# Kernel tuning notes

Measured on AMD Instinct MI355X. Metric: run time of the kernel, lower is better.

## Reference

```python
import jax, jax.numpy as jnp
import numpy as np

E = 8      # num routed experts
H = 1024   # hidden_size
I = 1408   # moe_intermediate_size
T = 2048   # tokens (batch*seq flattened)
K = 2      # top_k experts per token


def setup_inputs() -> dict:
    key = jax.random.key(0)
    k1, k2, k3, k4, k5 = jax.random.split(key, 5)
    x = jax.random.normal(k1, (T, H), dtype=jnp.float32)
    expert_ids = jax.random.randint(k2, (T, K), 0, E, dtype=jnp.int64)
    routing_weights = jax.random.uniform(k3, (T, K), dtype=jnp.float32)
    # kaiming_uniform_(a=sqrt(5)) on 2D tensor -> bound = 1/sqrt(fan_in), fan_in = dim1
    b1 = 1.0 / np.sqrt(2 * I)
    w1 = jax.random.uniform(k4, (E * H, 2 * I), dtype=jnp.float32, minval=-b1, maxval=b1)
    b2 = 1.0 / np.sqrt(H)
    w2 = jax.random.uniform(k5, (E * I, H), dtype=jnp.float32, minval=-b2, maxval=b2)
    return {"x": x, "expert_ids": expert_ids, "routing_weights": routing_weights,
            "w1": w1, "w2": w2}


def reference(x, expert_ids, routing_weights, w1, w2):
    # Fused routed MLP: per token, for each of its top-k experts e with gate p:
    #   out += p * (silu(x @ W1_gate[e]) * (x @ W1_up[e])) @ W2[e]
    w1r = w1.reshape(E, H, 2 * I)   # fused gate+up per expert
    w2r = w2.reshape(E, I, H)       # down proj per expert

    h = jnp.einsum('th,ehi->eti', x, w1r)           # [E, T, 2I]
    gate, up = h[..., :I], h[..., I:]
    act = jax.nn.silu(gate) * up                    # [E, T, I]
    y = jnp.einsum('eti,eih->eth', act, w2r)        # [E, T, H]

    # combine weights: [T, E] = sum over the k slots of onehot(expert)*routing_weight
    disp = jnp.sum(jax.nn.one_hot(expert_ids, E, dtype=x.dtype)
                   * routing_weights[..., None], axis=1)  # [T, E]
    out = jnp.einsum('eth,te->th', y, disp)         # [T, H]
    return out
```

## Files before the change

### kernel.cpp

```cpp
#include <hip/hip_runtime.h>
#include <hip/hip_bf16.h>
#include <math.h>

#define E    8
#define H    1024
#define I2   2816
#define II   1408
#define T    2048
#define KTOP 2
#define NP   (T * KTOP)

#define BM   128
#define BK   32
#define BNA  64
#define BN2  128
#define GX   40

#define CVT_BLKS  1024
#define W1_PER_E  (4 * 44)
#define W1_BLKS   (W1_PER_E * E)
#define W2_PER_E  (11 * 16)
#define W2_BLKS   (W2_PER_E * E)
#define PREP_BLKS (1 + CVT_BLKS + W1_BLKS + W2_BLKS)

typedef __attribute__((ext_vector_type(8))) short  short8v;
typedef __attribute__((ext_vector_type(4))) float  f32x4;
typedef __attribute__((ext_vector_type(8))) unsigned short ushort8;

__device__ __forceinline__ void gload16(void* lds, const void* g) {
    __builtin_amdgcn_global_load_lds((const __attribute__((address_space(1))) unsigned int*)g,
                                     (__attribute__((address_space(3))) unsigned int*)lds,
                                     16, 0, 0);
}

union PrepShared {
    char tiles[2][8192];
    struct { int cnt4[4][E]; int woff[4][E]; } rt;
};

__device__ __forceinline__ void tr_load(const float* __restrict__ src, int K, int N,
                                        int e, int n0, int krow0, int tid, float4* f)
{
    const float* s = src + (size_t)e * K * N + (size_t)(krow0 + (tid >> 2)) * N
                     + n0 + (tid & 3) * 16;
    f[0] = *(const float4*)(s);
    f[1] = *(const float4*)(s + 4);
    f[2] = *(const float4*)(s + 8);
    f[3] = *(const float4*)(s + 12);
}

__device__ __forceinline__ void tr_write(char* lds, int tid, const float4* f)
{
    alignas(16) __hip_bfloat16 t[16];
#pragma unroll
    for (int i = 0; i < 4; ++i) {
        t[4 * i + 0] = __float2bfloat16(f[i].x);
        t[4 * i + 1] = __float2bfloat16(f[i].y);
        t[4 * i + 2] = __float2bfloat16(f[i].z);
        t[4 * i + 3] = __float2bfloat16(f[i].w);
    }
    int r  = tid >> 2;
    int cb = (tid & 3) * 32;
    int sw = (r & 7) << 4;
    *(ushort8*)(lds + r * 128 + ((cb)      ^ sw)) = ((ushort8*)t)[0];
    *(ushort8*)(lds + r * 128 + ((cb + 16) ^ sw)) = ((ushort8*)t)[1];
}

__device__ __forceinline__ void tr_store(const char* lds0, const char* lds1,
                                         __hip_bfloat16* __restrict__ dst, int K, int N,
                                         int e, int n0, int kdst0, int tid)
{
    int g  = tid >> 7;
    int h  = tid & 127;
    int n  = h >> 1;
    int kb = 32 * (h & 1);
    const char* lds = g ? lds1 : lds0;
    alignas(16) __hip_bfloat16 t[32];
#pragma unroll
    for (int j = 0; j < 32; ++j) {
        int r = kb + j;
        t[j] = *(const __hip_bfloat16*)(lds + r * 128 + ((2 * n) ^ ((r & 7) << 4)));
    }
    __hip_bfloat16* d = dst + (size_t)e * K * N + (size_t)(n0 + n) * K + kdst0 + 64 * g + kb;
    *(ushort8*)(d)      = ((ushort8*)t)[0];
    *(ushort8*)(d + 8)  = ((ushort8*)t)[1];
    *(ushort8*)(d + 16) = ((ushort8*)t)[2];
    *(ushort8*)(d + 24) = ((ushort8*)t)[3];
}

__device__ __forceinline__ void tr_strip(const float* __restrict__ src,
                                         __hip_bfloat16* __restrict__ dst,
                                         int K, int N, int e, int n0, int k0,
                                         int np, PrepShared& sh, int tid)
{
    float4 fa0[4], fb0[4], fa1[4], fb1[4];
    tr_load(src, K, N, e, n0, k0,      tid, fa0);
    tr_load(src, K, N, e, n0, k0 + 64, tid, fb0);
    if (np == 2) {
        tr_load(src, K, N, e, n0, k0 + 128, tid, fa1);
        tr_load(src, K, N, e, n0, k0 + 192, tid, fb1);
    }
    tr_write(sh.tiles[0], tid, fa0);
    tr_write(sh.tiles[1], tid, fb0);
    __syncthreads();
    tr_store(sh.tiles[0], sh.tiles[1], dst, K, N, e, n0, k0, tid);
    if (np == 2) {
        __syncthreads();
        tr_write(sh.tiles[0], tid, fa1);
        tr_write(sh.tiles[1], tid, fb1);
        __syncthreads();
        tr_store(sh.tiles[0], sh.tiles[1], dst, K, N, e, n0, k0 + 128, tid);
    }
}

__launch_bounds__(256)
__global__ void prep_kernel(const float* __restrict__ x, const float* __restrict__ w1,
                            const float* __restrict__ w2, const int* __restrict__ ids,
                            __hip_bfloat16* __restrict__ xb,
                            __hip_bfloat16* __restrict__ w1t,
                            __hip_bfloat16* __restrict__ w2t,
                            int* __restrict__ tok, int* __restrict__ inv,
                            int* __restrict__ seg_off, int* __restrict__ tile_off)
{
    __shared__ PrepShared sh;
    int tid = threadIdx.x;
    int b = blockIdx.x;

    if (b == 0) {
        int lane = tid & 63;
        int w    = tid >> 6;
        unsigned long long ltm = (1ull << lane) - 1ull;

        int wc = 0;
#pragma unroll 1
        for (int it = 0; it < 16; ++it) {
            int p = it * 256 + w * 64 + lane;
            int e = ids[p];
#pragma unroll
            for (int ee = 0; ee < E; ++ee) {
                unsigned long long m = __ballot(e == ee);
                if (lane == ee) wc += (int)__popcll(m);
            }
        }
        if (lane < E) sh.rt.cnt4[w][lane] = wc;
        __syncthreads();
        if (tid == 0) {
            int base = 0, tiles = 0;
            for (int e = 0; e < E; ++e) {
                seg_off[e]  = base;
                tile_off[e] = tiles;
                int tot = 0;
                for (int ww = 0; ww < 4; ++ww) {
                    sh.rt.woff[ww][e] = base + tot;
                    tot += sh.rt.cnt4[ww][e];
                }
                base  += tot;
                tiles += (tot + BM - 1) / BM;
            }
            seg_off[E]  = base;
            tile_off[E] = tiles;
        }
        __syncthreads();
        int run = (lane < E) ? sh.rt.woff[w][lane] : 0;
#pragma unroll 1
        for (int it = 0; it < 16; ++it) {
            int p = it * 256 + w * 64 + lane;
            int e = ids[p];
            unsigned long long me = 0;
            int acnt = 0;
#pragma unroll
            for (int ee = 0; ee < E; ++ee) {
                unsigned long long m = __ballot(e == ee);
                if (e == ee) me = m;
                if (lane == ee) acnt = (int)__popcll(m);
            }
            int rank = (int)__popcll(me & ltm);
            int qb   = __shfl(run, e, 64);
            int q    = qb + rank;
            tok[q] = p >> 1;
            inv[p] = q;
            run += acnt;
        }
        return;
    }
    b -= 1;

    if (b < CVT_BLKS) {
        int i = (b * 256 + tid) * 8;
        float4 a = *(const float4*)(x + i);
        float4 c = *(const float4*)(x + i + 4);
        alignas(16) __hip_bfloat16 t[8];
        t[0] = __float2bfloat16(a.x); t[1] = __float2bfloat16(a.y);
        t[2] = __float2bfloat16(a.z); t[3] = __float2bfloat16(a.w);
        t[4] = __float2bfloat16(c.x); t[5] = __float2bfloat16(c.y);
        t[6] = __float2bfloat16(c.z); t[7] = __float2bfloat16(c.w);
        *(ushort8*)(xb + i) = *(ushort8*)t;
        return;
    }
    b -= CVT_BLKS;

    if (b < W1_BLKS) {
        int e = b / W1_PER_E, r = b % W1_PER_E;
        tr_strip(w1, w1t, H, I2, e, (r % 44) * 64, (r / 44) * 256, 2, sh, tid);
        return;
    }
    b -= W1_BLKS;
    {
        int e = b / W2_PER_E, r = b % W2_PER_E;
        tr_strip(w2, w2t, II, H, e, (r % 16) * 64, (r / 16) * 128, 1, sh, tid);
    }
}

__launch_bounds__(256, 2)
__global__ void gemm1_silu(const __hip_bfloat16* __restrict__ xb,
                           const __hip_bfloat16* __restrict__ w1t,
                           const int* __restrict__ tok,
                           const int* __restrict__ seg_off,
                           const int* __restrict__ tile_off,
                           __hip_bfloat16* __restrict__ act)
{
    __shared__ __align__(16) __hip_bfloat16 As[BM * BK];
    __shared__ __align__(16) __hip_bfloat16 Bg[BNA * BK];
    __shared__ __align__(16) __hip_bfloat16 Bu[BNA * BK];
    __shared__ int tokS[BM];

    int bx = blockIdx.x;
    if (bx >= tile_off[E]) return;
    int e = 0;
#pragma unroll
    for (int i = 1; i < E; ++i) if (bx >= tile_off[i]) e = i;
    int row0 = seg_off[e] + (bx - tile_off[e]) * BM;
    int rend = seg_off[e + 1];
    int jb   = blockIdx.y * BNA;

    int tid = threadIdx.x;
    if (tid < BM) {
        int gr = row0 + tid;
        tokS[tid] = tok[gr < NP ? gr : NP - 1];
    }
    __syncthreads();

    int arow = tid >> 2;
    int aoff = (tid & 3) * 16;
    const char* xB  = (const char*)xb;
    const char* w1B = (const char*)(w1t + (size_t)e * I2 * H);
    const char* srcA0 = xB + (size_t)tokS[arow]      * 2048 + aoff;
    const char* srcA1 = xB + (size_t)tokS[arow + 64] * 2048 + aoff;
    const char* srcG  = w1B + (size_t)(jb + arow)      * 2048 + aoff;
    const char* srcU  = w1B + (size_t)(II + jb + arow) * 2048 + aoff;
    __hip_bfloat16* dA0 = &As[tid * 8];
    __hip_bfloat16* dA1 = &As[2048 + tid * 8];
    __hip_bfloat16* dG  = &Bg[tid * 8];
    __hip_bfloat16* dU  = &Bu[tid * 8];

    int lane = tid & 63;
    int w  = tid >> 6;
    int wm = w >> 1, wn = w & 1;
    int fr = lane & 15;
    int kc = lane >> 4;

    f32x4 accg[4][2] = {};
    f32x4 accu[4][2] = {};
    const short8v* Asv = (const short8v*)As;
    const short8v* Bgv = (const short8v*)Bg;
    const short8v* Buv = (const short8v*)Bu;

    for (int k0 = 0; k0 < H; k0 += BK) {
        gload16(dA0, srcA0);
        gload16(dA1, srcA1);
        gload16(dG, srcG);
        gload16(dU, srcU);
        srcA0 += 64; srcA1 += 64; srcG += 64; srcU += 64;
        __syncthreads();

        short8v a[4], g[2], u[2];
#pragma unroll
        for (int m = 0; m < 4; ++m)
            a[m] = Asv[(wm * 64 + m * 16 + fr) * 4 + kc];
#pragma unroll
        for (int n = 0; n < 2; ++n) {
            g[n] = Bgv[(wn * 32 + n * 16 + fr) * 4 + kc];
            u[n] = Buv[(wn * 32 + n * 16 + fr) * 4 + kc];
        }
#pragma unroll
        for (int m = 0; m < 4; ++m)
#pragma unroll
            for (int n = 0; n < 2; ++n) {
                accg[m][n] = __builtin_amdgcn_mfma_f32_16x16x32_bf16(a[m], g[n], accg[m][n], 0, 0, 0);
                accu[m][n] = __builtin_amdgcn_mfma_f32_16x16x32_bf16(a[m], u[n], accu[m][n], 0, 0, 0);
            }
        __syncthreads();
    }

#pragma unroll
    for (int m = 0; m < 4; ++m)
#pragma unroll
        for (int n = 0; n < 2; ++n) {
            int col = jb + wn * 32 + n * 16 + fr;
#pragma unroll
            for (int j = 0; j < 4; ++j) {
                int gr = row0 + wm * 64 + m * 16 + kc * 4 + j;
                if (gr < rend) {
                    float gg = accg[m][n][j];
                    float s  = gg / (1.0f + __expf(-gg));
                    act[(size_t)gr * II + col] = __float2bfloat16(s * accu[m][n][j]);
                }
            }
        }
}

__launch_bounds__(256, 2)
__global__ void gemm2(const __hip_bfloat16* __restrict__ act,
                      const __hip_bfloat16* __restrict__ w2t,
                      const int* __restrict__ seg_off,
                      const int* __restrict__ tile_off,
                      float* __restrict__ y)
{
    __shared__ __align__(16) __hip_bfloat16 As[BM * BK];
    __shared__ __align__(16) __hip_bfloat16 Bs[BN2 * BK];

    int bx = blockIdx.x;
    if (bx >= tile_off[E]) return;
    int e = 0;
#pragma unroll
    for (int i = 1; i < E; ++i) if (bx >= tile_off[i]) e = i;
    int row0 = seg_off[e] + (bx - tile_off[e]) * BM;
    int rend = seg_off[e + 1];
    int nb   = blockIdx.y * BN2;

    int tid = threadIdx.x;
    int arow = tid >> 2;
    int aoff = (tid & 3) * 16;
    const char* actB = (const char*)act;
    const char* w2B  = (const char*)(w2t + (size_t)e * H * II);
    int r0c = row0 + arow;       r0c = r0c < NP ? r0c : NP - 1;
    int r1c = row0 + arow + 64;  r1c = r1c < NP ? r1c : NP - 1;
    const char* srcA0 = actB + (size_t)r0c * 2816 + aoff;
    const char* srcA1 = actB + (size_t)r1c * 2816 + aoff;
    const char* srcB0 = w2B + (size_t)(nb + arow)      * 2816 + aoff;
    const char* srcB1 = w2B + (size_t)(nb + arow + 64) * 2816 + aoff;
    __hip_bfloat16* dA0 = &As[tid * 8];
    __hip_bfloat16* dA1 = &As[2048 + tid * 8];
    __hip_bfloat16* dB0 = &Bs[tid * 8];
    __hip_bfloat16* dB1 = &Bs[2048 + tid * 8];

    int lane = tid & 63;
    int w  = tid >> 6;
    int wm = w >> 1, wn = w & 1;
    int fr = lane & 15;
    int kc = lane >> 4;

    f32x4 acc[4][4] = {};
    const short8v* Asv = (const short8v*)As;
    const short8v* Bsv = (const short8v*)Bs;

    for (int k0 = 0; k0 < II; k0 += BK) {
        gload16(dA0, srcA0);
        gload16(dA1, srcA1);
        gload16(dB0, srcB0);
        gload16(dB1, srcB1);
        srcA0 += 64; srcA1 += 64; srcB0 += 64; srcB1 += 64;
        __syncthreads();

        short8v a[4], b[4];
#pragma unroll
        for (int m = 0; m < 4; ++m)
            a[m] = Asv[(wm * 64 + m * 16 + fr) * 4 + kc];
#pragma unroll
        for (int n = 0; n < 4; ++n)
            b[n] = Bsv[(wn * 64 + n * 16 + fr) * 4 + kc];
#pragma unroll
        for (int m = 0; m < 4; ++m)
#pragma unroll
            for (int n = 0; n < 4; ++n)
                acc[m][n] = __builtin_amdgcn_mfma_f32_16x16x32_bf16(a[m], b[n], acc[m][n], 0, 0, 0);
        __syncthreads();
    }

#pragma unroll
    for (int m = 0; m < 4; ++m)
#pragma unroll
        for (int n = 0; n < 4; ++n) {
            int col = nb + wn * 64 + n * 16 + fr;
#pragma unroll
            for (int j = 0; j < 4; ++j) {
                int lr = wm * 64 + m * 16 + kc * 4 + j;
                int gr = row0 + lr;
                if (gr < rend)
                    y[(size_t)gr * H + col] = acc[m][n][j];
            }
        }
}

__global__ void gather_out(const float* __restrict__ y, const int* __restrict__ inv,
                           const float* __restrict__ rw, float* __restrict__ out)
{
    int gid = blockIdx.x * 256 + threadIdx.x;
    int t = gid >> 8;
    int c = (gid & 255) * 4;
    int q0 = inv[2 * t], q1 = inv[2 * t + 1];
    float w0 = rw[2 * t], w1 = rw[2 * t + 1];
    float4 a = *(const float4*)(y + (size_t)q0 * H + c);
    float4 b = *(const float4*)(y + (size_t)q1 * H + c);
    float4 o;
    o.x = w0 * a.x + w1 * b.x;
    o.y = w0 * a.y + w1 * b.y;
    o.z = w0 * a.z + w1 * b.z;
    o.w = w0 * a.w + w1 * b.w;
    *(float4*)(out + (size_t)t * H + c) = o;
}

extern "C" void kernel_launch(void* const* d_in, const int* in_sizes, int n_in,
                              void* d_out, int out_size, void* d_ws, size_t ws_size,
                              hipStream_t stream)
{
    const float* x   = (const float*)d_in[0];
    const int*   ids = (const int*)d_in[1];
    const float* rw  = (const float*)d_in[2];
    const float* w1  = (const float*)d_in[3];
    const float* w2  = (const float*)d_in[4];
    float*       out = (float*)d_out;

    char* ws = (char*)d_ws;
    int*   tok  = (int*)ws;
    int*   inv  = (int*)(ws + 16384);
    int*   seg  = (int*)(ws + 32768);
    int*   tile = (int*)(ws + 32768 + 64);
    __hip_bfloat16* xb  = (__hip_bfloat16*)(ws + 65536);
    __hip_bfloat16* w1t = (__hip_bfloat16*)(ws + 4259840);
    __hip_bfloat16* w2t = (__hip_bfloat16*)(ws + 50397184);
    __hip_bfloat16* act = (__hip_bfloat16*)(ws + 73465856);
    float*          y   = (float*)(ws + 85000192);

    prep_kernel<<<PREP_BLKS, 256, 0, stream>>>(x, w1, w2, ids, xb, w1t, w2t,
                                               tok, inv, seg, tile);

    gemm1_silu<<<dim3(GX, II / BNA), 256, 0, stream>>>(xb, w1t, tok, seg, tile, act);
    gemm2<<<dim3(GX, H / BN2), 256, 0, stream>>>(act, w2t, seg, tile, y);
    gather_out<<<(T * H) / (256 * 4), 256, 0, stream>>>(y, inv, rw, out);
}
```

Before: 286.1 us.

## Overlap W2 transpose with GEMM1 and use async LDS-loaded transpose tiles

Moves the W2 fp32-to-bf16 transpose out of the prep kernel and into extra blocks of the gemm1 launch, so that work can run alongside the first GEMM instead of before it. The transpose is also rewritten to load 64x64 fp32 tiles straight into LDS with global_load_lds and an XOR swizzle, then read out transposed. The W2 blocks share gemm1's LDS through a union, and each loops over several tiles. The risk is that these extra blocks compete with the GEMM blocks for CUs and bandwidth.

```diff
diff --git a/kernel.cpp b/kernel.cpp
--- a/kernel.cpp
+++ b/kernel.cpp
@@ -15,13 +15,15 @@
 #define BNA  64
 #define BN2  128
 #define GX   40
+#define GXT  8
 
 #define CVT_BLKS  1024
-#define W1_PER_E  (4 * 44)
-#define W1_BLKS   (W1_PER_E * E)
-#define W2_PER_E  (11 * 16)
-#define W2_BLKS   (W2_PER_E * E)
-#define PREP_BLKS (1 + CVT_BLKS + W1_BLKS + W2_BLKS)
+#define W1_TILES  (16 * 44 * E)
+#define PREP_BLKS (1 + CVT_BLKS + W1_TILES)
+
+#define W2_TILES     2816
+#define W2_BLOCKS    (GXT * 22)
+#define W2_PER_BLOCK (W2_TILES / W2_BLOCKS)
 
 typedef __attribute__((ext_vector_type(8))) short  short8v;
 typedef __attribute__((ext_vector_type(4))) float  f32x4;
@@ -33,96 +35,50 @@
                                      16, 0, 0);
 }
 
+__device__ __forceinline__ void transpose_tile_async(
+    const float* __restrict__ src, __hip_bfloat16* __restrict__ dst,
+    int K, int N, int k0, int n0, float* tile, int tid)
+{
+    int lane = tid & 63;
+    int wv   = tid >> 6;
+#pragma unroll
+    for (int i = 0; i < 4; ++i) {
+        int q   = (wv * 4 + i) * 64 + lane;
+        int r   = q >> 4;
+        int c16 = q & 15;
+        const float* gsrc = src + (size_t)(k0 + r) * N + n0 + ((c16 ^ (r & 15)) << 2);
+        gload16(tile + q * 4, gsrc);
+    }
+    __syncthreads();
+
+    int n  = tid >> 2;
+    int ks = (tid & 3) * 16;
+    alignas(16) __hip_bfloat16 t[16];
+#pragma unroll
+    for (int j = 0; j < 16; ++j) {
+        int r = ks + j;
+        float v = tile[r * 64 + (((n >> 2) ^ (r & 15)) << 2) + (n & 3)];
+        t[j] = __float2bfloat16(v);
+    }
+    __hip_bfloat16* d = dst + (size_t)(n0 + n) * K + k0 + ks;
+    *(ushort8*)(d)     = ((ushort8*)t)[0];
+    *(ushort8*)(d + 8) = ((ushort8*)t)[1];
+}
+
 union PrepShared {
-    char tiles[2][8192];
+    float tile[4096];
     struct { int cnt4[4][E]; int woff[4][E]; } rt;
 };
 
-__device__ __forceinline__ void tr_load(const float* __restrict__ src, int K, int N,
-                                        int e, int n0, int krow0, int tid, float4* f)
-{
-    const float* s = src + (size_t)e * K * N + (size_t)(krow0 + (tid >> 2)) * N
-                     + n0 + (tid & 3) * 16;
-    f[0] = *(const float4*)(s);
-    f[1] = *(const float4*)(s + 4);
-    f[2] = *(const float4*)(s + 8);
-    f[3] = *(const float4*)(s + 12);
-}
-
-__device__ __forceinline__ void tr_write(char* lds, int tid, const float4* f)
-{
-    alignas(16) __hip_bfloat16 t[16];
-#pragma unroll
-    for (int i = 0; i < 4; ++i) {
-        t[4 * i + 0] = __float2bfloat16(f[i].x);
-        t[4 * i + 1] = __float2bfloat16(f[i].y);
-        t[4 * i + 2] = __float2bfloat16(f[i].z);
-        t[4 * i + 3] = __float2bfloat16(f[i].w);
-    }
-    int r  = tid >> 2;
-    int cb = (tid & 3) * 32;
-    int sw = (r & 7) << 4;
-    *(ushort8*)(lds + r * 128 + ((cb)      ^ sw)) = ((ushort8*)t)[0];
-    *(ushort8*)(lds + r * 128 + ((cb + 16) ^ sw)) = ((ushort8*)t)[1];
-}
-
-__device__ __forceinline__ void tr_store(const char* lds0, const char* lds1,
-                                         __hip_bfloat16* __restrict__ dst, int K, int N,
-                                         int e, int n0, int kdst0, int tid)
-{
-    int g  = tid >> 7;
-    int h  = tid & 127;
-    int n  = h >> 1;
-    int kb = 32 * (h & 1);
-    const char* lds = g ? lds1 : lds0;
-    alignas(16) __hip_bfloat16 t[32];
-#pragma unroll
-    for (int j = 0; j < 32; ++j) {
-        int r = kb + j;
-        t[j] = *(const __hip_bfloat16*)(lds + r * 128 + ((2 * n) ^ ((r & 7) << 4)));
-    }
-    __hip_bfloat16* d = dst + (size_t)e * K * N + (size_t)(n0 + n) * K + kdst0 + 64 * g + kb;
-    *(ushort8*)(d)      = ((ushort8*)t)[0];
-    *(ushort8*)(d + 8)  = ((ushort8*)t)[1];
-    *(ushort8*)(d + 16) = ((ushort8*)t)[2];
-    *(ushort8*)(d + 24) = ((ushort8*)t)[3];
-}
-
-__device__ __forceinline__ void tr_strip(const float* __restrict__ src,
-                                         __hip_bfloat16* __restrict__ dst,
-                                         int K, int N, int e, int n0, int k0,
-                                         int np, PrepShared& sh, int tid)
-{
-    float4 fa0[4], fb0[4], fa1[4], fb1[4];
-    tr_load(src, K, N, e, n0, k0,      tid, fa0);
-    tr_load(src, K, N, e, n0, k0 + 64, tid, fb0);
-    if (np == 2) {
-        tr_load(src, K, N, e, n0, k0 + 128, tid, fa1);
-        tr_load(src, K, N, e, n0, k0 + 192, tid, fb1);
-    }
-    tr_write(sh.tiles[0], tid, fa0);
-    tr_write(sh.tiles[1], tid, fb0);
-    __syncthreads();
-    tr_store(sh.tiles[0], sh.tiles[1], dst, K, N, e, n0, k0, tid);
-    if (np == 2) {
-        __syncthreads();
-        tr_write(sh.tiles[0], tid, fa1);
-        tr_write(sh.tiles[1], tid, fb1);
-        __syncthreads();
-        tr_store(sh.tiles[0], sh.tiles[1], dst, K, N, e, n0, k0 + 128, tid);
-    }
-}
-
 __launch_bounds__(256)
 __global__ void prep_kernel(const float* __restrict__ x, const float* __restrict__ w1,
-                            const float* __restrict__ w2, const int* __restrict__ ids,
+                            const int* __restrict__ ids,
                             __hip_bfloat16* __restrict__ xb,
                             __hip_bfloat16* __restrict__ w1t,
-                            __hip_bfloat16* __restrict__ w2t,
                             int* __restrict__ tok, int* __restrict__ inv,
                             int* __restrict__ seg_off, int* __restrict__ tile_off)
 {
-    __shared__ PrepShared sh;
+    __shared__ __align__(16) PrepShared sh;
     int tid = threadIdx.x;
     int b = blockIdx.x;
 
@@ -199,32 +155,52 @@
     }
     b -= CVT_BLKS;
 
-    if (b < W1_BLKS) {
-        int e = b / W1_PER_E, r = b % W1_PER_E;
-        tr_strip(w1, w1t, H, I2, e, (r % 44) * 64, (r / 44) * 256, 2, sh, tid);
-        return;
-    }
-    b -= W1_BLKS;
     {
-        int e = b / W2_PER_E, r = b % W2_PER_E;
-        tr_strip(w2, w2t, II, H, e, (r % 16) * 64, (r / 16) * 128, 1, sh, tid);
-    }
-}
+        int e = b / 704, r = b % 704;
+        int k0 = (r / 44) * 64, n0 = (r % 44) * 64;
+        transpose_tile_async(w1 + (size_t)e * H * I2, w1t + (size_t)e * I2 * H,
+                             H, I2, k0, n0, sh.tile, tid);
+    }
+}
+
+union Gemm1Shared {
+    struct {
+        __hip_bfloat16 As[BM * BK];
+        __hip_bfloat16 Bg[BNA * BK];
+        __hip_bfloat16 Bu[BNA * BK];
+        int tokS[BM];
+    } g;
+    float tile[4096];
+};
 
 __launch_bounds__(256, 2)
 __global__ void gemm1_silu(const __hip_bfloat16* __restrict__ xb,
                            const __hip_bfloat16* __restrict__ w1t,
+                           const float* __restrict__ w2,
+                           __hip_bfloat16* __restrict__ w2t,
                            const int* __restrict__ tok,
                            const int* __restrict__ seg_off,
                            const int* __restrict__ tile_off,
                            __hip_bfloat16* __restrict__ act)
 {
-    __shared__ __align__(16) __hip_bfloat16 As[BM * BK];
-    __shared__ __align__(16) __hip_bfloat16 Bg[BNA * BK];
-    __shared__ __align__(16) __hip_bfloat16 Bu[BNA * BK];
-    __shared__ int tokS[BM];
-
+    __shared__ __align__(16) Gemm1Shared sh;
+    int tid = threadIdx.x;
     int bx = blockIdx.x;
+
+    if (bx >= GX) {
+        int wid = (bx - GX) * 22 + blockIdx.y;
+#pragma unroll 1
+        for (int i = 0; i < W2_PER_BLOCK; ++i) {
+            int t = wid * W2_PER_BLOCK + i;
+            int e = t / 352, r = t % 352;
+            int k0 = (r >> 4) * 64, n0 = (r & 15) * 64;
+            transpose_tile_async(w2 + (size_t)e * II * H, w2t + (size_t)e * H * II,
+                                 II, H, k0, n0, sh.tile, tid);
+            __syncthreads();
+        }
+        return;
+    }
+
     if (bx >= tile_off[E]) return;
     int e = 0;
 #pragma unroll
@@ -233,10 +209,13 @@
     int rend = seg_off[e + 1];
     int jb   = blockIdx.y * BNA;
 
-    int tid = threadIdx.x;
+    __hip_bfloat16* As = sh.g.As;
+    __hip_bfloat16* Bg = sh.g.Bg;
+    __hip_bfloat16* Bu = sh.g.Bu;
+
     if (tid < BM) {
         int gr = row0 + tid;
-        tokS[tid] = tok[gr < NP ? gr : NP - 1];
+        sh.g.tokS[tid] = tok[gr < NP ? gr : NP - 1];
     }
     __syncthreads();
 
@@ -244,8 +223,8 @@
     int aoff = (tid & 3) * 16;
     const char* xB  = (const char*)xb;
     const char* w1B = (const char*)(w1t + (size_t)e * I2 * H);
-    const char* srcA0 = xB + (size_t)tokS[arow]      * 2048 + aoff;
-    const char* srcA1 = xB + (size_t)tokS[arow + 64] * 2048 + aoff;
+    const char* srcA0 = xB + (size_t)sh.g.tokS[arow]      * 2048 + aoff;
+    const char* srcA1 = xB + (size_t)sh.g.tokS[arow + 64] * 2048 + aoff;
     const char* srcG  = w1B + (size_t)(jb + arow)      * 2048 + aoff;
     const char* srcU  = w1B + (size_t)(II + jb + arow) * 2048 + aoff;
     __hip_bfloat16* dA0 = &As[tid * 8];
@@ -432,10 +411,10 @@
     __hip_bfloat16* act = (__hip_bfloat16*)(ws + 73465856);
     float*          y   = (float*)(ws + 85000192);
 
-    prep_kernel<<<PREP_BLKS, 256, 0, stream>>>(x, w1, w2, ids, xb, w1t, w2t,
-                                               tok, inv, seg, tile);
-
-    gemm1_silu<<<dim3(GX, II / BNA), 256, 0, stream>>>(xb, w1t, tok, seg, tile, act);
+    prep_kernel<<<PREP_BLKS, 256, 0, stream>>>(x, w1, ids, xb, w1t, tok, inv, seg, tile);
+
+    gemm1_silu<<<dim3(GX + GXT, II / BNA), 256, 0, stream>>>(xb, w1t, w2, w2t,
+                                                             tok, seg, tile, act);
     gemm2<<<dim3(GX, H / BN2), 256, 0, stream>>>(act, w2t, seg, tile, y);
     gather_out<<<(T * H) / (256 * 4), 256, 0, stream>>>(y, inv, rw, out);
 }
```

Result: no change. 285.3 us (-0.3%).
